# Optimization experiments

Hardware: AMD Instinct MI355X
Metric: run time of the kernel (lower is better)

## Reference

```python
import jax, jax.numpy as jnp
import numpy as np

VOCAB = 10000
EMB = 256
FILTERS = 256
KS = [2, 3, 4]
NUM_LABELS = 6
B, L = 4, 256


def _conv1d_same(x, w, b, k):
    # x: [B, C, L], w: [O, I, k] -> [B, O, L]; torch 'same' pad: left=(k-1)//2
    pad_l = (k - 1) // 2
    pad_r = (k - 1) - pad_l
    y = jax.lax.conv_general_dilated(
        x, w, window_strides=(1,), padding=[(pad_l, pad_r)],
        dimension_numbers=('NCH', 'OIH', 'NCH'))
    return y + b[None, :, None]


def setup_inputs() -> dict:
    key = jax.random.key(0)
    ks = jax.random.split(key, 12)
    s = 0.02
    return {
        'input_ids': jax.random.randint(ks[0], (B, L), 0, VOCAB),
        'emb_table': jax.random.normal(ks[1], (VOCAB, EMB), jnp.float32) * s,
        'w2': jax.random.normal(ks[2], (FILTERS, EMB, 2), jnp.float32) * s,
        'b2': jax.random.normal(ks[3], (FILTERS,), jnp.float32) * s,
        'w3': jax.random.normal(ks[4], (FILTERS, EMB, 3), jnp.float32) * s,
        'b3': jax.random.normal(ks[5], (FILTERS,), jnp.float32) * s,
        'w4': jax.random.normal(ks[6], (FILTERS, EMB, 4), jnp.float32) * s,
        'b4': jax.random.normal(ks[7], (FILTERS,), jnp.float32) * s,
        'triple_w': jax.random.normal(ks[8], (NUM_LABELS, 3 * FILTERS), jnp.float32) * s,
        'triple_b': jax.random.normal(ks[9], (NUM_LABELS,), jnp.float32) * s,
        'score_w': jax.random.normal(ks[10], (1, 3 * FILTERS), jnp.float32) * s,
        'score_b': jax.random.normal(ks[11], (1,), jnp.float32) * s,
    }


def reference(input_ids, emb_table, w2, b2, w3, b3, w4, b4,
              triple_w, triple_b, score_w, score_b):
    emb = emb_table[input_ids]              # [B, L, E]
    x = jnp.transpose(emb, (0, 2, 1))       # [B, E, L]
    outs = [_conv1d_same(x, w, b, k) for (w, b, k)
            in ((w2, b2, 2), (w3, b3, 3), (w4, b4, 4))]
    out = jnp.concatenate(outs, axis=1)     # [B, 3F, L]
    out = jnp.transpose(out, (0, 2, 1))     # [B, L, K], K = 3F
    # dropout is identity in eval mode
    pair = jnp.einsum('bik,bjk->bijk', out, out)          # [B, L, L, K]
    triple_logits = jnp.einsum('bijk,ck->bijc', pair, triple_w) + triple_b
    scores = jnp.einsum('bijk,ck->bijc', pair, score_w) + score_b
    scores = scores[..., 0]                 # squeeze(-1) -> [B, L, L]
    return triple_logits, scores
```

## Files before the change

kernel.cpp:

```cpp
#include <hip/hip_runtime.h>
#include <stdint.h>

#define LSEQ 256
#define EMB  256
#define K3F  768
#define SCOFF (4 * 256 * 256 * 6)

typedef short bf16x8 __attribute__((ext_vector_type(8)));
typedef float f32x4  __attribute__((ext_vector_type(4)));

__device__ __forceinline__ uint16_t f2bf(float x) {
    union { float f; uint32_t u; } c; c.f = x;
    uint32_t r = c.u + 0x7fffu + ((c.u >> 16) & 1u);
    return (uint16_t)(r >> 16);
}

__device__ __forceinline__ uint32_t scale_pk(uint32_t u, float t0, float t1) {
    union { uint32_t u; float f; } lo, hi;
    lo.u = u << 16;
    hi.u = u & 0xffff0000u;
    float a = lo.f * t0;
    float b = hi.f * t1;
    return (uint32_t)f2bf(a) | ((uint32_t)f2bf(b) << 16);
}

__global__ __launch_bounds__(256) void k_prep(const int* __restrict__ ids,
                                              const float* __restrict__ table,
                                              const float* __restrict__ w2,
                                              const float* __restrict__ w3,
                                              const float* __restrict__ w4,
                                              uint16_t* __restrict__ embB,
                                              uint16_t* __restrict__ Wt2,
                                              uint16_t* __restrict__ Wt3,
                                              uint16_t* __restrict__ Wt4) {
    int blk = blockIdx.x, tid = threadIdx.x;
    if (blk < 32) {
        int b = blk >> 3, l0 = (blk & 7) << 5;
        int r = tid >> 3, p = tid & 7;
        int id = ids[(b << 8) + l0 + r];
        const float* src = table + (size_t)id * EMB + p * 32;
        uint16_t* dst = embB + (size_t)(b * 272 + 4 + l0 + r) * 256 + p * 32;
#pragma unroll
        for (int s = 0; s < 8; ++s) {
            float4 v = *(const float4*)(src + 4 * s);
            uint32_t lo = f2bf(v.x) | ((uint32_t)f2bf(v.y) << 16);
            uint32_t hi = f2bf(v.z) | ((uint32_t)f2bf(v.w) << 16);
            *(uint2*)(dst + 4 * s) = make_uint2(lo, hi);
        }
    } else if (blk < 36) {
        int b = blk - 32;
        int ri = tid >> 4;
        int row = ri < 4 ? ri : 256 + ri;
        int off = (tid & 15) * 16;
        uint16_t* dst = embB + (size_t)(b * 272 + row) * 256 + off;
        *(uint4*)dst = make_uint4(0, 0, 0, 0);
        *(uint4*)(dst + 8) = make_uint4(0, 0, 0, 0);
    } else {
        int n = (blk - 36) * 256 + tid;
        if (n < 65536) {
            int c = n >> 8, i = n & 255;
            float2 v = *(const float2*)(w2 + (c << 9) + (i << 1));
            Wt2[c * 256 + i]         = f2bf(v.x);
            Wt2[65536 + c * 256 + i] = f2bf(v.y);
        } else if (n < 131072) {
            int m = n - 65536;
            int c = m >> 8, i = m & 255;
            const float* s = w3 + c * 768 + i * 3;
#pragma unroll
            for (int t = 0; t < 3; ++t)
                Wt3[t * 65536 + c * 256 + i] = f2bf(s[t]);
        } else {
            int m = n - 131072;
            int c = m >> 8, i = m & 255;
            float4 v = *(const float4*)(w4 + (c << 10) + (i << 2));
            Wt4[c * 256 + i]              = f2bf(v.x);
            Wt4[65536 + c * 256 + i]      = f2bf(v.y);
            Wt4[2 * 65536 + c * 256 + i]  = f2bf(v.z);
            Wt4[3 * 65536 + c * 256 + i]  = f2bf(v.w);
        }
    }
}

template <int K, int PAD>
__device__ __forceinline__ void convg_body(const uint16_t* __restrict__ Wt,
                                           const float* __restrict__ bias,
                                           const uint16_t* __restrict__ embB,
                                           uint16_t* __restrict__ VB,
                                           int b, int c0, int l0, int gbase,
                                           uint16_t (*As)[32][72], uint16_t (*Bs)[72]) {
    const int tid = threadIdx.x;
    const int lane = tid & 63, wave = tid >> 6;
    const int ms = wave >> 1, ns = wave & 1;
    const int m = lane & 15, q = lane >> 4;
    const int ar = tid >> 3, aseg = (tid & 7) * 8;

    const uint16_t* wsrc  = Wt + (size_t)(c0 + ar) * 256 + aseg;
    const uint16_t* bsrc  = embB + (size_t)(b * 272 + 3 + l0 + ar) * 256 + aseg;
    const int r2 = 32 + (tid >> 3);
    const uint16_t* bsrc2 = embB + (size_t)(b * 272 + 3 + l0 + r2) * 256 + aseg;

    bf16x8 ra[K], rb, rb2;
#pragma unroll
    for (int t = 0; t < K; ++t) ra[t] = *(const bf16x8*)(wsrc + t * 65536);
    rb = *(const bf16x8*)bsrc;
    if (tid < 32) rb2 = *(const bf16x8*)bsrc2;

    f32x4 acc;
#pragma unroll
    for (int z = 0; z < 4; ++z) acc[z] = 0.f;

#pragma unroll
    for (int i0 = 0; i0 < EMB; i0 += 64) {
        __syncthreads();
#pragma unroll
        for (int t = 0; t < K; ++t) *(bf16x8*)&As[t][ar][aseg] = ra[t];
        *(bf16x8*)&Bs[ar][aseg] = rb;
        if (tid < 32) *(bf16x8*)&Bs[r2][aseg] = rb2;
        __syncthreads();
        if (i0 + 64 < EMB) {
#pragma unroll
            for (int t = 0; t < K; ++t) ra[t] = *(const bf16x8*)(wsrc + t * 65536 + i0 + 64);
            rb = *(const bf16x8*)(bsrc + i0 + 64);
            if (tid < 32) rb2 = *(const bf16x8*)(bsrc2 + i0 + 64);
        }
#pragma unroll
        for (int t = 0; t < K; ++t) {
#pragma unroll
            for (int kh = 0; kh < 64; kh += 32) {
                bf16x8 afr = *(const bf16x8*)&As[t][ms * 16 + m][kh + q * 8];
                bf16x8 bfr = *(const bf16x8*)&Bs[ns * 16 + m + t - PAD + 1][kh + q * 8];
                acc = __builtin_amdgcn_mfma_f32_16x16x32_bf16(afr, bfr, acc, 0, 0, 0);
            }
        }
    }
    __syncthreads();
    float (*Cs)[36] = (float(*)[36])As;
#pragma unroll
    for (int rg = 0; rg < 4; ++rg)
        Cs[ms * 16 + q * 4 + rg][ns * 16 + m] = acc[rg];
    __syncthreads();
    const int l = tid >> 3, cs = (tid & 7) * 4;
    const float4 bv = *(const float4*)(bias + c0 + cs);
    union { uint16_t h[4]; uint32_t d[2]; } pk;
    pk.h[0] = f2bf(Cs[cs + 0][l] + bv.x);
    pk.h[1] = f2bf(Cs[cs + 1][l] + bv.y);
    pk.h[2] = f2bf(Cs[cs + 2][l] + bv.z);
    pk.h[3] = f2bf(Cs[cs + 3][l] + bv.w);
    uint16_t* vdst = VB + (size_t)(b * 256 + l0 + l) * K3F + gbase + c0 + cs;
    *(uint2*)vdst = make_uint2(pk.d[0], pk.d[1]);
}

__global__ __launch_bounds__(256, 4) void k_convg(const uint16_t* __restrict__ Wt2,
                                                  const uint16_t* __restrict__ Wt3,
                                                  const uint16_t* __restrict__ Wt4,
                                                  const float* __restrict__ b2,
                                                  const float* __restrict__ b3,
                                                  const float* __restrict__ b4,
                                                  const uint16_t* __restrict__ embB,
                                                  uint16_t* __restrict__ VB) {
    __shared__ __align__(16) uint16_t As[4][32][72];
    __shared__ __align__(16) uint16_t Bs[36][72];
    int blk = blockIdx.x;
    int b = blk & 3, rest = blk >> 2;
    int g = rest >> 6, rr = rest & 63;
    int c0 = (rr >> 3) * 32, l0 = (rr & 7) * 32;
    if (g == 0)      convg_body<2, 0>(Wt2, b2, embB, VB, b, c0, l0, 0,   As, Bs);
    else if (g == 1) convg_body<3, 1>(Wt3, b3, embB, VB, b, c0, l0, 256, As, Bs);
    else             convg_body<4, 1>(Wt4, b4, embB, VB, b, c0, l0, 512, As, Bs);
}

__global__ __launch_bounds__(256, 4) void k_pairc2(const uint16_t* __restrict__ VB,
                                                   const float* __restrict__ tw,
                                                   const float* __restrict__ sw,
                                                   const float* __restrict__ tb,
                                                   const float* __restrict__ sb,
                                                   float* __restrict__ dout) {
    __shared__ __align__(16) uint16_t T[96][136];
    __shared__ __align__(16) float twL[768];
    int blk = blockIdx.x;
    int b = blk & 3, it = (blk >> 2) & 7;
    int rest = blk >> 5;
    int c = rest % 7, jp = rest / 7;
    int i0 = it * 32, j0 = jp * 64;
    int tid = threadIdx.x;

    const float* srow = (c < 6) ? (tw + c * K3F) : sw;
    twL[tid]       = srow[tid];
    twL[256 + tid] = srow[256 + tid];
    twL[512 + tid] = srow[512 + tid];

    int lane = tid & 63, wave = tid >> 6;
    int iw = wave >> 1, jw = wave & 1;
    int m = lane & 15, q = lane >> 4;
    int rr = tid >> 3, seg = (tid & 7) * 16;

    const uint16_t* srcI  = VB + (size_t)(b * 256 + i0 + rr) * K3F + seg;
    const uint16_t* srcJ0 = VB + (size_t)(b * 256 + j0 + rr) * K3F + seg;
    const uint16_t* srcJ1 = VB + (size_t)(b * 256 + j0 + 32 + rr) * K3F + seg;

    bf16x8 rI0, rI1, rJ00, rJ01, rJ10, rJ11;
    rI0  = *(const bf16x8*)(srcI);      rI1  = *(const bf16x8*)(srcI + 8);
    rJ00 = *(const bf16x8*)(srcJ0);     rJ01 = *(const bf16x8*)(srcJ0 + 8);
    rJ10 = *(const bf16x8*)(srcJ1);     rJ11 = *(const bf16x8*)(srcJ1 + 8);

    f32x4 acc[2];
#pragma unroll
    for (int n = 0; n < 2; ++n)
#pragma unroll
        for (int z = 0; z < 4; ++z) acc[n][z] = 0.f;

#pragma unroll
    for (int kc = 0; kc < K3F; kc += 128) {
        __syncthreads();
        {
            const float* twp = twL + kc + seg;
            float4 t0 = *(const float4*)(twp + 0);
            float4 t1 = *(const float4*)(twp + 4);
            float4 t2 = *(const float4*)(twp + 8);
            float4 t3 = *(const float4*)(twp + 12);
            union { bf16x8 v; uint32_t u[4]; } a0, a1, r0, r1;
            a0.v = rI0; a1.v = rI1;
            r0.u[0] = scale_pk(a0.u[0], t0.x, t0.y);
            r0.u[1] = scale_pk(a0.u[1], t0.z, t0.w);
            r0.u[2] = scale_pk(a0.u[2], t1.x, t1.y);
            r0.u[3] = scale_pk(a0.u[3], t1.z, t1.w);
            r1.u[0] = scale_pk(a1.u[0], t2.x, t2.y);
            r1.u[1] = scale_pk(a1.u[1], t2.z, t2.w);
            r1.u[2] = scale_pk(a1.u[2], t3.x, t3.y);
            r1.u[3] = scale_pk(a1.u[3], t3.z, t3.w);
            *(bf16x8*)&T[rr][seg]     = r0.v;
            *(bf16x8*)&T[rr][seg + 8] = r1.v;
        }
        *(bf16x8*)&T[32 + rr][seg]     = rJ00;
        *(bf16x8*)&T[32 + rr][seg + 8] = rJ01;
        *(bf16x8*)&T[64 + rr][seg]     = rJ10;
        *(bf16x8*)&T[64 + rr][seg + 8] = rJ11;
        __syncthreads();
        if (kc + 128 < K3F) {
            rI0  = *(const bf16x8*)(srcI + kc + 128);
            rI1  = *(const bf16x8*)(srcI + kc + 136);
            rJ00 = *(const bf16x8*)(srcJ0 + kc + 128);
            rJ01 = *(const bf16x8*)(srcJ0 + kc + 136);
            rJ10 = *(const bf16x8*)(srcJ1 + kc + 128);
            rJ11 = *(const bf16x8*)(srcJ1 + kc + 136);
        }
#pragma unroll
        for (int kh = 0; kh < 4; ++kh) {
            bf16x8 afr  = *(const bf16x8*)&T[iw * 16 + m][kh * 32 + q * 8];
            bf16x8 bfr0 = *(const bf16x8*)&T[32 + jw * 32 + m][kh * 32 + q * 8];
            bf16x8 bfr1 = *(const bf16x8*)&T[32 + jw * 32 + 16 + m][kh * 32 + q * 8];
            acc[0] = __builtin_amdgcn_mfma_f32_16x16x32_bf16(afr, bfr0, acc[0], 0, 0, 0);
            acc[1] = __builtin_amdgcn_mfma_f32_16x16x32_bf16(afr, bfr1, acc[1], 0, 0, 0);
        }
    }
    float bias = (c < 6) ? tb[c] : sb[0];
#pragma unroll
    for (int n = 0; n < 2; ++n)
#pragma unroll
        for (int rg = 0; rg < 4; ++rg) {
            int i = i0 + iw * 16 + q * 4 + rg;
            int j = j0 + jw * 32 + n * 16 + m;
            float v = acc[n][rg] + bias;
            if (c < 6) dout[((size_t)(b * 256 + i) * 256 + j) * 6 + c] = v;
            else       dout[SCOFF + (size_t)(b * 256 + i) * 256 + j] = v;
        }
}

extern "C" void kernel_launch(void* const* d_in, const int* in_sizes, int n_in,
                              void* d_out, int out_size, void* d_ws, size_t ws_size,
                              hipStream_t stream) {
    const int*   ids   = (const int*)d_in[0];
    const float* table = (const float*)d_in[1];
    const float* w2 = (const float*)d_in[2];
    const float* b2 = (const float*)d_in[3];
    const float* w3 = (const float*)d_in[4];
    const float* b3 = (const float*)d_in[5];
    const float* w4 = (const float*)d_in[6];
    const float* b4 = (const float*)d_in[7];
    const float* tw = (const float*)d_in[8];
    const float* tb = (const float*)d_in[9];
    const float* sw = (const float*)d_in[10];
    const float* sb = (const float*)d_in[11];
    float* dout = (float*)d_out;

    uint8_t* wsb = (uint8_t*)d_ws;
    uint16_t* VB   = (uint16_t*)(wsb + 0);
    uint16_t* embB = (uint16_t*)(wsb + 1572864);
    uint16_t* Wt2  = (uint16_t*)(wsb + 2129920);
    uint16_t* Wt3  = (uint16_t*)(wsb + 2392064);
    uint16_t* Wt4  = (uint16_t*)(wsb + 2785280);

    hipLaunchKernelGGL(k_prep,   dim3(804), dim3(256), 0, stream,
                       ids, table, w2, w3, w4, embB, Wt2, Wt3, Wt4);
    hipLaunchKernelGGL(k_convg,  dim3(768), dim3(256), 0, stream,
                       Wt2, Wt3, Wt4, b2, b3, b4, embB, VB);
    hipLaunchKernelGGL(k_pairc2, dim3(896), dim3(256), 0, stream,
                       VB, tw, sw, tb, sb, dout);
}
```

Measured before the change: 106.8 us.

## Fuse embedding gather and weight bf16 conversion into conv kernel, drop prep kernel

```diff
diff --git a/kernel.cpp b/kernel.cpp
--- a/kernel.cpp
+++ b/kernel.cpp
@@ -15,76 +15,22 @@
     return (uint16_t)(r >> 16);
 }
 
+__device__ __forceinline__ uint32_t pk2(float a, float b) {
+    return (uint32_t)f2bf(a) | ((uint32_t)f2bf(b) << 16);
+}
+
 __device__ __forceinline__ uint32_t scale_pk(uint32_t u, float t0, float t1) {
     union { uint32_t u; float f; } lo, hi;
     lo.u = u << 16;
     hi.u = u & 0xffff0000u;
-    float a = lo.f * t0;
-    float b = hi.f * t1;
-    return (uint32_t)f2bf(a) | ((uint32_t)f2bf(b) << 16);
-}
-
-__global__ __launch_bounds__(256) void k_prep(const int* __restrict__ ids,
-                                              const float* __restrict__ table,
-                                              const float* __restrict__ w2,
-                                              const float* __restrict__ w3,
-                                              const float* __restrict__ w4,
-                                              uint16_t* __restrict__ embB,
-                                              uint16_t* __restrict__ Wt2,
-                                              uint16_t* __restrict__ Wt3,
-                                              uint16_t* __restrict__ Wt4) {
-    int blk = blockIdx.x, tid = threadIdx.x;
-    if (blk < 32) {
-        int b = blk >> 3, l0 = (blk & 7) << 5;
-        int r = tid >> 3, p = tid & 7;
-        int id = ids[(b << 8) + l0 + r];
-        const float* src = table + (size_t)id * EMB + p * 32;
-        uint16_t* dst = embB + (size_t)(b * 272 + 4 + l0 + r) * 256 + p * 32;
-#pragma unroll
-        for (int s = 0; s < 8; ++s) {
-            float4 v = *(const float4*)(src + 4 * s);
-            uint32_t lo = f2bf(v.x) | ((uint32_t)f2bf(v.y) << 16);
-            uint32_t hi = f2bf(v.z) | ((uint32_t)f2bf(v.w) << 16);
-            *(uint2*)(dst + 4 * s) = make_uint2(lo, hi);
-        }
-    } else if (blk < 36) {
-        int b = blk - 32;
-        int ri = tid >> 4;
-        int row = ri < 4 ? ri : 256 + ri;
-        int off = (tid & 15) * 16;
-        uint16_t* dst = embB + (size_t)(b * 272 + row) * 256 + off;
-        *(uint4*)dst = make_uint4(0, 0, 0, 0);
-        *(uint4*)(dst + 8) = make_uint4(0, 0, 0, 0);
-    } else {
-        int n = (blk - 36) * 256 + tid;
-        if (n < 65536) {
-            int c = n >> 8, i = n & 255;
-            float2 v = *(const float2*)(w2 + (c << 9) + (i << 1));
-            Wt2[c * 256 + i]         = f2bf(v.x);
-            Wt2[65536 + c * 256 + i] = f2bf(v.y);
-        } else if (n < 131072) {
-            int m = n - 65536;
-            int c = m >> 8, i = m & 255;
-            const float* s = w3 + c * 768 + i * 3;
-#pragma unroll
-            for (int t = 0; t < 3; ++t)
-                Wt3[t * 65536 + c * 256 + i] = f2bf(s[t]);
-        } else {
-            int m = n - 131072;
-            int c = m >> 8, i = m & 255;
-            float4 v = *(const float4*)(w4 + (c << 10) + (i << 2));
-            Wt4[c * 256 + i]              = f2bf(v.x);
-            Wt4[65536 + c * 256 + i]      = f2bf(v.y);
-            Wt4[2 * 65536 + c * 256 + i]  = f2bf(v.z);
-            Wt4[3 * 65536 + c * 256 + i]  = f2bf(v.w);
-        }
-    }
+    return pk2(lo.f * t0, hi.f * t1);
 }
 
 template <int K, int PAD>
-__device__ __forceinline__ void convg_body(const uint16_t* __restrict__ Wt,
+__device__ __forceinline__ void convg_body(const float* __restrict__ W,
                                            const float* __restrict__ bias,
-                                           const uint16_t* __restrict__ embB,
+                                           const int* __restrict__ ids,
+                                           const float* __restrict__ table,
                                            uint16_t* __restrict__ VB,
                                            int b, int c0, int l0, int gbase,
                                            uint16_t (*As)[32][72], uint16_t (*Bs)[72]) {
@@ -94,16 +40,28 @@
     const int m = lane & 15, q = lane >> 4;
     const int ar = tid >> 3, aseg = (tid & 7) * 8;
 
-    const uint16_t* wsrc  = Wt + (size_t)(c0 + ar) * 256 + aseg;
-    const uint16_t* bsrc  = embB + (size_t)(b * 272 + 3 + l0 + ar) * 256 + aseg;
+    const int l1 = l0 + ar - 1;
+    const int id1 = (l1 >= 0 && l1 < 256) ? ids[(b << 8) + l1] : -1;
+    const float* bsrc = table + (size_t)(id1 < 0 ? 0 : id1) * 256 + aseg;
     const int r2 = 32 + (tid >> 3);
-    const uint16_t* bsrc2 = embB + (size_t)(b * 272 + 3 + l0 + r2) * 256 + aseg;
-
-    bf16x8 ra[K], rb, rb2;
-#pragma unroll
-    for (int t = 0; t < K; ++t) ra[t] = *(const bf16x8*)(wsrc + t * 65536);
-    rb = *(const bf16x8*)bsrc;
-    if (tid < 32) rb2 = *(const bf16x8*)bsrc2;
+    const int l2 = l0 + r2 - 1;
+    const int id2 = (tid < 32 && l2 < 256) ? ids[(b << 8) + l2] : -1;
+    const float* bsrc2 = table + (size_t)(id2 < 0 ? 0 : id2) * 256 + aseg;
+
+    union { float4 v[2 * K]; float f[8 * K]; } rw;
+    float4 rb[2], rb2[2];
+
+    {
+        const float* wp = W + ((size_t)(c0 + ar) * 256 + aseg) * K;
+#pragma unroll
+        for (int u = 0; u < 2 * K; ++u) rw.v[u] = *(const float4*)(wp + 4 * u);
+        rb[0] = *(const float4*)(bsrc);
+        rb[1] = *(const float4*)(bsrc + 4);
+        if (tid < 32) {
+            rb2[0] = *(const float4*)(bsrc2);
+            rb2[1] = *(const float4*)(bsrc2 + 4);
+        }
+    }
 
     f32x4 acc;
 #pragma unroll
@@ -112,16 +70,43 @@
 #pragma unroll
     for (int i0 = 0; i0 < EMB; i0 += 64) {
         __syncthreads();
-#pragma unroll
-        for (int t = 0; t < K; ++t) *(bf16x8*)&As[t][ar][aseg] = ra[t];
-        *(bf16x8*)&Bs[ar][aseg] = rb;
-        if (tid < 32) *(bf16x8*)&Bs[r2][aseg] = rb2;
+        {
+#pragma unroll
+            for (int t = 0; t < K; ++t) {
+                uint32_t d0 = pk2(rw.f[0 * K + t], rw.f[1 * K + t]);
+                uint32_t d1 = pk2(rw.f[2 * K + t], rw.f[3 * K + t]);
+                uint32_t d2 = pk2(rw.f[4 * K + t], rw.f[5 * K + t]);
+                uint32_t d3 = pk2(rw.f[6 * K + t], rw.f[7 * K + t]);
+                *(uint4*)&As[t][ar][aseg] = make_uint4(d0, d1, d2, d3);
+            }
+        }
+        {
+            uint4 bw;
+            if (id1 >= 0) {
+                bw = make_uint4(pk2(rb[0].x, rb[0].y), pk2(rb[0].z, rb[0].w),
+                                pk2(rb[1].x, rb[1].y), pk2(rb[1].z, rb[1].w));
+            } else bw = make_uint4(0, 0, 0, 0);
+            *(uint4*)&Bs[ar][aseg] = bw;
+            if (tid < 32) {
+                uint4 bw2;
+                if (id2 >= 0) {
+                    bw2 = make_uint4(pk2(rb2[0].x, rb2[0].y), pk2(rb2[0].z, rb2[0].w),
+                                     pk2(rb2[1].x, rb2[1].y), pk2(rb2[1].z, rb2[1].w));
+                } else bw2 = make_uint4(0, 0, 0, 0);
+                *(uint4*)&Bs[r2][aseg] = bw2;
+            }
+        }
         __syncthreads();
         if (i0 + 64 < EMB) {
-#pragma unroll
-            for (int t = 0; t < K; ++t) ra[t] = *(const bf16x8*)(wsrc + t * 65536 + i0 + 64);
-            rb = *(const bf16x8*)(bsrc + i0 + 64);
-            if (tid < 32) rb2 = *(const bf16x8*)(bsrc2 + i0 + 64);
+            const float* wp = W + ((size_t)(c0 + ar) * 256 + i0 + 64 + aseg) * K;
+#pragma unroll
+            for (int u = 0; u < 2 * K; ++u) rw.v[u] = *(const float4*)(wp + 4 * u);
+            rb[0] = *(const float4*)(bsrc + i0 + 64);
+            rb[1] = *(const float4*)(bsrc + i0 + 68);
+            if (tid < 32) {
+                rb2[0] = *(const float4*)(bsrc2 + i0 + 64);
+                rb2[1] = *(const float4*)(bsrc2 + i0 + 68);
+            }
         }
 #pragma unroll
         for (int t = 0; t < K; ++t) {
@@ -150,13 +135,14 @@
     *(uint2*)vdst = make_uint2(pk.d[0], pk.d[1]);
 }
 
-__global__ __launch_bounds__(256, 4) void k_convg(const uint16_t* __restrict__ Wt2,
-                                                  const uint16_t* __restrict__ Wt3,
-                                                  const uint16_t* __restrict__ Wt4,
+__global__ __launch_bounds__(256, 4) void k_convg(const float* __restrict__ w2,
+                                                  const float* __restrict__ w3,
+                                                  const float* __restrict__ w4,
                                                   const float* __restrict__ b2,
                                                   const float* __restrict__ b3,
                                                   const float* __restrict__ b4,
-                                                  const uint16_t* __restrict__ embB,
+                                                  const int* __restrict__ ids,
+                                                  const float* __restrict__ table,
                                                   uint16_t* __restrict__ VB) {
     __shared__ __align__(16) uint16_t As[4][32][72];
     __shared__ __align__(16) uint16_t Bs[36][72];
@@ -164,9 +150,9 @@
     int b = blk & 3, rest = blk >> 2;
     int g = rest >> 6, rr = rest & 63;
     int c0 = (rr >> 3) * 32, l0 = (rr & 7) * 32;
-    if (g == 0)      convg_body<2, 0>(Wt2, b2, embB, VB, b, c0, l0, 0,   As, Bs);
-    else if (g == 1) convg_body<3, 1>(Wt3, b3, embB, VB, b, c0, l0, 256, As, Bs);
-    else             convg_body<4, 1>(Wt4, b4, embB, VB, b, c0, l0, 512, As, Bs);
+    if (g == 0)      convg_body<2, 0>(w2, b2, ids, table, VB, b, c0, l0, 0,   As, Bs);
+    else if (g == 1) convg_body<3, 1>(w3, b3, ids, table, VB, b, c0, l0, 256, As, Bs);
+    else             convg_body<4, 1>(w4, b4, ids, table, VB, b, c0, l0, 512, As, Bs);
 }
 
 __global__ __launch_bounds__(256, 4) void k_pairc2(const uint16_t* __restrict__ VB,
@@ -283,17 +269,10 @@
     const float* sb = (const float*)d_in[11];
     float* dout = (float*)d_out;
 
-    uint8_t* wsb = (uint8_t*)d_ws;
-    uint16_t* VB   = (uint16_t*)(wsb + 0);
-    uint16_t* embB = (uint16_t*)(wsb + 1572864);
-    uint16_t* Wt2  = (uint16_t*)(wsb + 2129920);
-    uint16_t* Wt3  = (uint16_t*)(wsb + 2392064);
-    uint16_t* Wt4  = (uint16_t*)(wsb + 2785280);
-
-    hipLaunchKernelGGL(k_prep,   dim3(804), dim3(256), 0, stream,
-                       ids, table, w2, w3, w4, embB, Wt2, Wt3, Wt4);
+    uint16_t* VB = (uint16_t*)d_ws;
+
     hipLaunchKernelGGL(k_convg,  dim3(768), dim3(256), 0, stream,
-                       Wt2, Wt3, Wt4, b2, b3, b4, embB, VB);
+                       w2, w3, w4, b2, b3, b4, ids, table, VB);
     hipLaunchKernelGGL(k_pairc2, dim3(896), dim3(256), 0, stream,
                        VB, tw, sw, tb, sb, dout);
 }
```

Result: slower. 109.8 us (+2.8%).

## Enlarge pair-contraction tile to 64x64 with 2x2 MFMA per wave

Applied to the files above, without the earlier changes.

```diff
diff --git a/kernel.cpp b/kernel.cpp
--- a/kernel.cpp
+++ b/kernel.cpp
@@ -169,101 +169,97 @@
     else             convg_body<4, 1>(Wt4, b4, embB, VB, b, c0, l0, 512, As, Bs);
 }
 
-__global__ __launch_bounds__(256, 4) void k_pairc2(const uint16_t* __restrict__ VB,
+__global__ __launch_bounds__(256, 4) void k_pairc3(const uint16_t* __restrict__ VB,
                                                    const float* __restrict__ tw,
                                                    const float* __restrict__ sw,
                                                    const float* __restrict__ tb,
                                                    const float* __restrict__ sb,
                                                    float* __restrict__ dout) {
-    __shared__ __align__(16) uint16_t T[96][136];
-    __shared__ __align__(16) float twL[768];
+    __shared__ __align__(16) uint16_t T[128][136];
     int blk = blockIdx.x;
-    int b = blk & 3, it = (blk >> 2) & 7;
-    int rest = blk >> 5;
-    int c = rest % 7, jp = rest / 7;
-    int i0 = it * 32, j0 = jp * 64;
+    int b = blk & 3, r = blk >> 2;
+    int it = r & 3; r >>= 2;
+    int jp = r & 3; int c = r >> 2;
+    int i0 = it * 64, j0 = jp * 64;
     int tid = threadIdx.x;
 
-    const float* srow = (c < 6) ? (tw + c * K3F) : sw;
-    twL[tid]       = srow[tid];
-    twL[256 + tid] = srow[256 + tid];
-    twL[512 + tid] = srow[512 + tid];
-
     int lane = tid & 63, wave = tid >> 6;
-    int iw = wave >> 1, jw = wave & 1;
+    int iw = (wave >> 1) * 32, jw = (wave & 1) * 32;
     int m = lane & 15, q = lane >> 4;
-    int rr = tid >> 3, seg = (tid & 7) * 16;
-
-    const uint16_t* srcI  = VB + (size_t)(b * 256 + i0 + rr) * K3F + seg;
-    const uint16_t* srcJ0 = VB + (size_t)(b * 256 + j0 + rr) * K3F + seg;
-    const uint16_t* srcJ1 = VB + (size_t)(b * 256 + j0 + 32 + rr) * K3F + seg;
-
-    bf16x8 rI0, rI1, rJ00, rJ01, rJ10, rJ11;
-    rI0  = *(const bf16x8*)(srcI);      rI1  = *(const bf16x8*)(srcI + 8);
-    rJ00 = *(const bf16x8*)(srcJ0);     rJ01 = *(const bf16x8*)(srcJ0 + 8);
-    rJ10 = *(const bf16x8*)(srcJ1);     rJ11 = *(const bf16x8*)(srcJ1 + 8);
-
-    f32x4 acc[2];
-#pragma unroll
-    for (int n = 0; n < 2; ++n)
-#pragma unroll
-        for (int z = 0; z < 4; ++z) acc[n][z] = 0.f;
+    int ar = tid >> 2, aseg = (tid & 3) * 32;
+
+    const uint16_t* srcA = VB + (size_t)(b * 256 + i0 + ar) * K3F + aseg;
+    const uint16_t* srcB = VB + (size_t)(b * 256 + j0 + ar) * K3F + aseg;
+    const float*    srcT = ((c < 6) ? (tw + c * K3F) : sw) + aseg;
+
+    bf16x8 rA[4], rB[4];
+    float4 rT[8];
+#pragma unroll
+    for (int p = 0; p < 4; ++p) {
+        rA[p] = *(const bf16x8*)(srcA + p * 8);
+        rB[p] = *(const bf16x8*)(srcB + p * 8);
+        rT[2 * p]     = *(const float4*)(srcT + p * 8);
+        rT[2 * p + 1] = *(const float4*)(srcT + p * 8 + 4);
+    }
+
+    f32x4 acc[2][2];
+#pragma unroll
+    for (int a = 0; a < 2; ++a)
+#pragma unroll
+        for (int n = 0; n < 2; ++n)
+#pragma unroll
+            for (int z = 0; z < 4; ++z) acc[a][n][z] = 0.f;
 
 #pragma unroll
     for (int kc = 0; kc < K3F; kc += 128) {
         __syncthreads();
-        {
-            const float* twp = twL + kc + seg;
-            float4 t0 = *(const float4*)(twp + 0);
-            float4 t1 = *(const float4*)(twp + 4);
-            float4 t2 = *(const float4*)(twp + 8);
-            float4 t3 = *(const float4*)(twp + 12);
-            union { bf16x8 v; uint32_t u[4]; } a0, a1, r0, r1;
-            a0.v = rI0; a1.v = rI1;
+#pragma unroll
+        for (int p = 0; p < 4; ++p) {
+            union { bf16x8 v; uint32_t u[4]; } a0, r0;
+            a0.v = rA[p];
+            float4 t0 = rT[2 * p], t1 = rT[2 * p + 1];
             r0.u[0] = scale_pk(a0.u[0], t0.x, t0.y);
             r0.u[1] = scale_pk(a0.u[1], t0.z, t0.w);
             r0.u[2] = scale_pk(a0.u[2], t1.x, t1.y);
             r0.u[3] = scale_pk(a0.u[3], t1.z, t1.w);
-            r1.u[0] = scale_pk(a1.u[0], t2.x, t2.y);
-            r1.u[1] = scale_pk(a1.u[1], t2.z, t2.w);
-            r1.u[2] = scale_pk(a1.u[2], t3.x, t3.y);
-            r1.u[3] = scale_pk(a1.u[3], t3.z, t3.w);
-            *(bf16x8*)&T[rr][seg]     = r0.v;
-            *(bf16x8*)&T[rr][seg + 8] = r1.v;
-        }
-        *(bf16x8*)&T[32 + rr][seg]     = rJ00;
-        *(bf16x8*)&T[32 + rr][seg + 8] = rJ01;
-        *(bf16x8*)&T[64 + rr][seg]     = rJ10;
-        *(bf16x8*)&T[64 + rr][seg + 8] = rJ11;
+            *(bf16x8*)&T[ar][aseg + p * 8]      = r0.v;
+            *(bf16x8*)&T[64 + ar][aseg + p * 8] = rB[p];
+        }
         __syncthreads();
         if (kc + 128 < K3F) {
-            rI0  = *(const bf16x8*)(srcI + kc + 128);
-            rI1  = *(const bf16x8*)(srcI + kc + 136);
-            rJ00 = *(const bf16x8*)(srcJ0 + kc + 128);
-            rJ01 = *(const bf16x8*)(srcJ0 + kc + 136);
-            rJ10 = *(const bf16x8*)(srcJ1 + kc + 128);
-            rJ11 = *(const bf16x8*)(srcJ1 + kc + 136);
+#pragma unroll
+            for (int p = 0; p < 4; ++p) {
+                rA[p] = *(const bf16x8*)(srcA + kc + 128 + p * 8);
+                rB[p] = *(const bf16x8*)(srcB + kc + 128 + p * 8);
+                rT[2 * p]     = *(const float4*)(srcT + kc + 128 + p * 8);
+                rT[2 * p + 1] = *(const float4*)(srcT + kc + 132 + p * 8);
+            }
         }
 #pragma unroll
         for (int kh = 0; kh < 4; ++kh) {
-            bf16x8 afr  = *(const bf16x8*)&T[iw * 16 + m][kh * 32 + q * 8];
-            bf16x8 bfr0 = *(const bf16x8*)&T[32 + jw * 32 + m][kh * 32 + q * 8];
-            bf16x8 bfr1 = *(const bf16x8*)&T[32 + jw * 32 + 16 + m][kh * 32 + q * 8];
-            acc[0] = __builtin_amdgcn_mfma_f32_16x16x32_bf16(afr, bfr0, acc[0], 0, 0, 0);
-            acc[1] = __builtin_amdgcn_mfma_f32_16x16x32_bf16(afr, bfr1, acc[1], 0, 0, 0);
+            bf16x8 af0 = *(const bf16x8*)&T[iw + m][kh * 32 + q * 8];
+            bf16x8 af1 = *(const bf16x8*)&T[iw + 16 + m][kh * 32 + q * 8];
+            bf16x8 bf0 = *(const bf16x8*)&T[64 + jw + m][kh * 32 + q * 8];
+            bf16x8 bf1 = *(const bf16x8*)&T[64 + jw + 16 + m][kh * 32 + q * 8];
+            acc[0][0] = __builtin_amdgcn_mfma_f32_16x16x32_bf16(af0, bf0, acc[0][0], 0, 0, 0);
+            acc[0][1] = __builtin_amdgcn_mfma_f32_16x16x32_bf16(af0, bf1, acc[0][1], 0, 0, 0);
+            acc[1][0] = __builtin_amdgcn_mfma_f32_16x16x32_bf16(af1, bf0, acc[1][0], 0, 0, 0);
+            acc[1][1] = __builtin_amdgcn_mfma_f32_16x16x32_bf16(af1, bf1, acc[1][1], 0, 0, 0);
         }
     }
     float bias = (c < 6) ? tb[c] : sb[0];
 #pragma unroll
-    for (int n = 0; n < 2; ++n)
-#pragma unroll
-        for (int rg = 0; rg < 4; ++rg) {
-            int i = i0 + iw * 16 + q * 4 + rg;
-            int j = j0 + jw * 32 + n * 16 + m;
-            float v = acc[n][rg] + bias;
-            if (c < 6) dout[((size_t)(b * 256 + i) * 256 + j) * 6 + c] = v;
-            else       dout[SCOFF + (size_t)(b * 256 + i) * 256 + j] = v;
-        }
+    for (int a = 0; a < 2; ++a)
+#pragma unroll
+        for (int n = 0; n < 2; ++n)
+#pragma unroll
+            for (int rg = 0; rg < 4; ++rg) {
+                int i = i0 + iw + a * 16 + q * 4 + rg;
+                int j = j0 + jw + n * 16 + m;
+                float v = acc[a][n][rg] + bias;
+                if (c < 6) dout[((size_t)(b * 256 + i) * 256 + j) * 6 + c] = v;
+                else       dout[SCOFF + (size_t)(b * 256 + i) * 256 + j] = v;
+            }
 }
 
 extern "C" void kernel_launch(void* const* d_in, const int* in_sizes, int n_in,
@@ -294,6 +290,6 @@
                        ids, table, w2, w3, w4, embB, Wt2, Wt3, Wt4);
     hipLaunchKernelGGL(k_convg,  dim3(768), dim3(256), 0, stream,
                        Wt2, Wt3, Wt4, b2, b3, b4, embB, VB);
-    hipLaunchKernelGGL(k_pairc2, dim3(896), dim3(256), 0, stream,
+    hipLaunchKernelGGL(k_pairc3, dim3(448), dim3(256), 0, stream,
                        VB, tw, sw, tb, sb, dout);
 }
```

Measured after the change: 115.6 us. +8.2%, slower.
